# Optimization experiments

Hardware: AMD Instinct MI355X
Metric: run time of the kernel (lower is better)

The kernel has to match this reference:

```python
import jax, jax.numpy as jnp
import numpy as np

K = 2  # kernel_size


def setup_inputs() -> dict:
    key = jax.random.key(0)
    k1, k2, k3, k4, k5 = jax.random.split(key, 5)
    B, C, H, W_sp = 8, 256, 128, 128
    N = 512                      # number of keypoints
    E = C * K * K                # embed_dim = 1024
    img_feat_highres = jax.random.normal(k1, (B, C, H, W_sp), dtype=jnp.float32)
    W = jax.random.normal(k2, (E, C, K, K), dtype=jnp.float32) * 0.02  # conv weight, OIHW
    b = jax.random.normal(k3, (E,), dtype=jnp.float32) * 0.02          # conv bias
    batch_indices = jnp.broadcast_to(jnp.arange(B, dtype=jnp.int64)[:, None], (B, N))
    pixel_x_id = jax.random.randint(k4, (B, N), 0, H // 2, dtype=jnp.int64)  # low-res ids
    pixel_y_id = jax.random.randint(k5, (B, N), 0, H // 2, dtype=jnp.int64)
    return {
        "img_feat_highres": img_feat_highres,
        "W": W,
        "b": b,
        "batch_indices": batch_indices,
        "pixel_x_id": pixel_x_id,
        "pixel_y_id": pixel_y_id,
    }


def reference(img_feat_highres, W, b, batch_indices, pixel_x_id, pixel_y_id):
    # Dense conv2d, stride 1, padding = K-1 (torch nn.Conv2d semantics)
    patches = jax.lax.conv_general_dilated(
        img_feat_highres, W,
        window_strides=(1, 1),
        padding=((K - 1, K - 1), (K - 1, K - 1)),
        dimension_numbers=("NCHW", "OIHW", "NCHW"),
    ) + b[None, :, None, None]  # (B, E, H+K-1, W+K-1)

    y0 = 2 * pixel_y_id  # (B, N)
    x0 = 2 * pixel_x_id

    def samp(dy, dx):
        # advanced indices at dims 0,2,3 (non-adjacent) -> result (B, N, E)
        return patches[batch_indices, :, y0 + dy, x0 + dx]

    local_feat = jnp.concatenate(
        [samp(0, 0), samp(K, 0), samp(0, K), samp(K, K)], axis=2
    )  # (B, N, 4E)
    return jnp.transpose(local_feat, (0, 2, 1))  # (B, 4E, N)
```

## Files before the change

kernel.cpp:

```cpp
#include <hip/hip_runtime.h>
#include <stdint.h>


typedef __attribute__((ext_vector_type(8))) short bf16x8;
typedef __attribute__((ext_vector_type(4))) float f32x4;

#define GAS(p) ((const __attribute__((address_space(1))) void*)(p))
#define LAS(p) ((__attribute__((address_space(3))) void*)(p))

__device__ __forceinline__ unsigned short f2bf(float f) {
    union { float f; uint32_t u; } x; x.f = f;
    uint32_t u = x.u;
    uint32_t r = (u + 0x7FFFu + ((u >> 16) & 1u)) >> 16;
    return (unsigned short)r;
}

__global__ __launch_bounds__(256)
void prep_kernel(const float* __restrict__ img, const float* __restrict__ Wf,
                 unsigned short* __restrict__ Wp, unsigned short* __restrict__ zp,
                 unsigned short* __restrict__ imgT) {
    __shared__ unsigned short sT[8192];
    const int blk = blockIdx.x;
    const int t = threadIdx.x;

    if (blk < 1024) {
        const int e = blk, c = t;
        float4 w4 = *(const float4*)&Wf[(size_t)e * 1024 + c * 4];
        Wp[e * 1024 + 0 * 256 + c] = f2bf(w4.x);
        Wp[e * 1024 + 1 * 256 + c] = f2bf(w4.y);
        Wp[e * 1024 + 2 * 256 + c] = f2bf(w4.z);
        Wp[e * 1024 + 3 * 256 + c] = f2bf(w4.w);
        if (e == 0 && c < 32) {
            uint4 z = {0, 0, 0, 0};
            ((uint4*)zp)[c] = z;
        }
        return;
    }

    const int ib = blk - 1024;
    const int cc = ib & 3;
    const int y  = (ib >> 2) & 127;
    const int b  = ib >> 9;
    const int xq = t & 31;
    const int ch = t >> 5;
    unsigned int* sU = (unsigned int*)sT;
    const size_t pl = ((size_t)b * 256 + cc * 64) * 16384 + (size_t)y * 128;
    #pragma unroll
    for (int it = 0; it < 4; ++it) {
        const int cp = it * 8 + ch;
        const float4 v0 = *(const float4*)&img[pl + (size_t)(2 * cp)     * 16384 + xq * 4];
        const float4 v1 = *(const float4*)&img[pl + (size_t)(2 * cp + 1) * 16384 + xq * 4];
        const float a0[4] = {v0.x, v0.y, v0.z, v0.w};
        const float a1[4] = {v1.x, v1.y, v1.z, v1.w};
        #pragma unroll
        for (int j = 0; j < 4; ++j) {
            const int x = xq * 4 + j;
            const unsigned int pk = (unsigned)f2bf(a0[j]) | ((unsigned)f2bf(a1[j]) << 16);
            sU[x * 32 + (cp ^ (x & 31))] = pk;
        }
    }
    __syncthreads();
    unsigned short* ob = imgT + (((size_t)b * 128 + y) * 128) * 256 + cc * 64;
    #pragma unroll
    for (int jj = 0; jj < 16; ++jj) {
        const int oo = t + 256 * jj;
        const int xx = oo >> 5;
        const int c2 = oo & 31;
        const unsigned int pk = sU[xx * 32 + (c2 ^ (xx & 31))];
        *(unsigned int*)&ob[(size_t)xx * 256 + c2 * 2] = pk;
    }
}

__global__ __launch_bounds__(256)
void gemm_kernel(const unsigned short* __restrict__ Wp,
                 const unsigned short* __restrict__ imgT,
                 const unsigned short* __restrict__ zp,
                 const int* __restrict__ bidx,
                 const int* __restrict__ pxid,
                 const int* __restrict__ pyid,
                 const float* __restrict__ bias,
                 float* __restrict__ out) {
    const int orig = blockIdx.x;
    const int wg = (orig & 7) * 128 + (orig >> 3);
    const int et = wg & 7;
    const int nt = wg >> 3;
    const int g  = nt >> 2;
    const int n0 = (nt & 3) * 128;
    const int e0 = et * 128;
    const int b = g >> 2, o = g & 3;

    const int tid  = threadIdx.x;
    const int lane = tid & 63;
    const int wid  = tid >> 6;
    const int wr   = wid >> 1;
    const int wc   = wid & 1;

    __shared__ unsigned short sW[2][8192];
    __shared__ unsigned short sA[2][8192];

    const int row0 = tid >> 3;
    const int cg   = (tid & 7) ^ (row0 & 7);
    int ay[4], ax[4];
    size_t apl[4];
    #pragma unroll
    for (int r = 0; r < 4; ++r) {
        const int row = row0 + 32 * r;
        const int gi = b * 512 + n0 + row;
        apl[r] = (size_t)bidx[gi] * (128 * 128 * 256);
        ay[r] = 2 * pyid[gi] - 1 + (o & 1) * 2;
        ax[r] = 2 * pxid[gi] - 1 + (o >> 1) * 2;
    }

    const f32x4 fzero = {0.f, 0.f, 0.f, 0.f};
    f32x4 acc[4][4];
    #pragma unroll
    for (int m = 0; m < 4; ++m)
        #pragma unroll
        for (int nf = 0; nf < 4; ++nf) acc[m][nf] = fzero;

    auto stage = [&](int kc, int buf) {
        const int p   = kc >> 2;
        const int csh = (kc & 3) * 64;
        #pragma unroll
        for (int r = 0; r < 4; ++r) {
            const int i   = r * 256 + tid;
            const int row = row0 + 32 * r;
            const unsigned short* gw = Wp + (size_t)(e0 + row) * 1024 + kc * 64 + cg * 8;
            __builtin_amdgcn_global_load_lds(GAS(gw), LAS(&sW[buf][i * 8]), 16, 0, 0);
            const int yy = ay[r] + (p >> 1);
            const int xx = ax[r] + (p & 1);
            const unsigned short* ga =
                ((unsigned)yy < 128u && (unsigned)xx < 128u)
                    ? imgT + apl[r] + ((size_t)(yy * 128 + xx)) * 256 + csh + cg * 8
                    : zp + cg * 8;
            __builtin_amdgcn_global_load_lds(GAS(ga), LAS(&sA[buf][i * 8]), 16, 0, 0);
        }
    };

    stage(0, 0);
    stage(1, 1);
    for (int kt = 0; kt < 16; ++kt) {
        const int cur = kt & 1;
        if (kt == 15) { asm volatile("s_waitcnt vmcnt(0)" ::: "memory"); }
        else          { asm volatile("s_waitcnt vmcnt(8)" ::: "memory"); }
        __builtin_amdgcn_s_barrier();

        #pragma unroll
        for (int ks = 0; ks < 2; ++ks) {
            bf16x8 af[4], bfr[4];
            #pragma unroll
            for (int m = 0; m < 4; ++m) {
                const int row = wr * 64 + m * 16 + (lane & 15);
                const int cl  = (ks * 4 + (lane >> 4)) ^ (row & 7);
                af[m] = *(const bf16x8*)&sW[cur][row * 64 + cl * 8];
            }
            #pragma unroll
            for (int nf = 0; nf < 4; ++nf) {
                const int row = wc * 64 + nf * 16 + (lane & 15);
                const int cl  = (ks * 4 + (lane >> 4)) ^ (row & 7);
                bfr[nf] = *(const bf16x8*)&sA[cur][row * 64 + cl * 8];
            }
            __builtin_amdgcn_s_setprio(1);
            #pragma unroll
            for (int m = 0; m < 4; ++m)
                #pragma unroll
                for (int nf = 0; nf < 4; ++nf)
                    acc[m][nf] = __builtin_amdgcn_mfma_f32_16x16x32_bf16(
                        af[m], bfr[nf], acc[m][nf], 0, 0, 0);
            __builtin_amdgcn_s_setprio(0);
        }

        __builtin_amdgcn_s_barrier();
        if (kt + 2 < 16) stage(kt + 2, cur);
    }

    const int erow_l = (lane >> 4) * 4;
    const int ncol_l = lane & 15;
    #pragma unroll
    for (int m = 0; m < 4; ++m) {
        #pragma unroll
        for (int nf = 0; nf < 4; ++nf) {
            const int nn = n0 + wc * 64 + nf * 16 + ncol_l;
            #pragma unroll
            for (int reg = 0; reg < 4; ++reg) {
                const int e = e0 + wr * 64 + m * 16 + erow_l + reg;
                out[((size_t)g * 1024 + e) * 512 + nn] = acc[m][nf][reg] + bias[e];
            }
        }
    }
}

extern "C" void kernel_launch(void* const* d_in, const int* in_sizes, int n_in,
                              void* d_out, int out_size, void* d_ws, size_t ws_size,
                              hipStream_t stream) {
    const float* img  = (const float*)d_in[0];
    const float* Wf   = (const float*)d_in[1];
    const float* bias = (const float*)d_in[2];
    const int*   bidx = (const int*)d_in[3];
    const int*   pxid = (const int*)d_in[4];
    const int*   pyid = (const int*)d_in[5];
    float* out = (float*)d_out;

    unsigned short* Wp   = (unsigned short*)((char*)d_ws + (32u << 20));
    unsigned short* zp   = (unsigned short*)((char*)d_ws + (36u << 20));
    unsigned short* imgT = (unsigned short*)((char*)d_ws + (64u << 20));

    hipLaunchKernelGGL(prep_kernel, dim3(5120), dim3(256), 0, stream,
                       img, Wf, Wp, zp, imgT);
    hipLaunchKernelGGL(gemm_kernel, dim3(1024), dim3(256), 0, stream,
                       Wp, imgT, zp, bidx, pxid, pyid, bias, out);
}
```

Before: 84.22 us.

## Enlarge GEMM tiles to 256x256 with 512 threads and pre-swizzled weights

The gather-GEMM kernel now uses 256x256 output tiles with 8 waves, which halves the grid to 256 blocks and increases data reuse per block. The prep kernel writes the weights in a pre-tiled, swizzled bf16 layout so each block loads them with contiguous direct-to-LDS copies. The K loop is split into half-stages, and each barrier immediately issues the next half's loads for finer-grained double buffering. The larger accumulator array raises register pressure, and only 256 blocks may underfill the GPU.

```diff
diff --git a/kernel.cpp b/kernel.cpp
--- a/kernel.cpp
+++ b/kernel.cpp
@@ -17,32 +17,46 @@
 
 __global__ __launch_bounds__(256)
 void prep_kernel(const float* __restrict__ img, const float* __restrict__ Wf,
-                 unsigned short* __restrict__ Wp, unsigned short* __restrict__ zp,
+                 unsigned short* __restrict__ Wq, unsigned short* __restrict__ zp,
                  unsigned short* __restrict__ imgT) {
     __shared__ unsigned short sT[8192];
     const int blk = blockIdx.x;
-    const int t = threadIdx.x;
-
-    if (blk < 1024) {
-        const int e = blk, c = t;
-        float4 w4 = *(const float4*)&Wf[(size_t)e * 1024 + c * 4];
-        Wp[e * 1024 + 0 * 256 + c] = f2bf(w4.x);
-        Wp[e * 1024 + 1 * 256 + c] = f2bf(w4.y);
-        Wp[e * 1024 + 2 * 256 + c] = f2bf(w4.z);
-        Wp[e * 1024 + 3 * 256 + c] = f2bf(w4.w);
-        if (e == 0 && c < 32) {
+    const int tid = threadIdx.x;
+
+    if (blk < 512) {
+        if (blk == 0 && tid < 32) {
             uint4 z = {0, 0, 0, 0};
-            ((uint4*)zp)[c] = z;
-        }
+            ((uint4*)zp)[tid] = z;
+        }
+        const int t  = blk * 256 + tid;
+        const int et = t >> 15;
+        const int r1 = t & 32767;
+        const int j  = r1 >> 11;
+        const int r2 = r1 & 2047;
+        const int h  = r2 >> 10;
+        const int r3 = r2 & 1023;
+        const int chunk = r3 >> 8;
+        const int row   = r3 & 255;
+        const int e  = et * 256 + row;
+        const int kb = j * 64 + h * 32 + chunk * 8;
+        unsigned short v[8];
+        #pragma unroll
+        for (int kk = 0; kk < 8; ++kk) {
+            const int k = kb + kk;
+            const int c = k & 255;
+            const int p = k >> 8;
+            v[kk] = f2bf(Wf[(size_t)e * 1024 + c * 4 + p]);
+        }
+        *(uint4*)&Wq[(size_t)t * 8] = *(const uint4*)v;
         return;
     }
 
-    const int ib = blk - 1024;
+    const int ib = blk - 512;
     const int cc = ib & 3;
     const int y  = (ib >> 2) & 127;
     const int b  = ib >> 9;
-    const int xq = t & 31;
-    const int ch = t >> 5;
+    const int xq = tid & 31;
+    const int ch = tid >> 5;
     unsigned int* sU = (unsigned int*)sT;
     const size_t pl = ((size_t)b * 256 + cc * 64) * 16384 + (size_t)y * 128;
     #pragma unroll
@@ -53,9 +67,9 @@
         const float a0[4] = {v0.x, v0.y, v0.z, v0.w};
         const float a1[4] = {v1.x, v1.y, v1.z, v1.w};
         #pragma unroll
-        for (int j = 0; j < 4; ++j) {
-            const int x = xq * 4 + j;
-            const unsigned int pk = (unsigned)f2bf(a0[j]) | ((unsigned)f2bf(a1[j]) << 16);
+        for (int jj = 0; jj < 4; ++jj) {
+            const int x = xq * 4 + jj;
+            const unsigned int pk = (unsigned)f2bf(a0[jj]) | ((unsigned)f2bf(a1[jj]) << 16);
             sU[x * 32 + (cp ^ (x & 31))] = pk;
         }
     }
@@ -63,7 +77,7 @@
     unsigned short* ob = imgT + (((size_t)b * 128 + y) * 128) * 256 + cc * 64;
     #pragma unroll
     for (int jj = 0; jj < 16; ++jj) {
-        const int oo = t + 256 * jj;
+        const int oo = tid + 256 * jj;
         const int xx = oo >> 5;
         const int c2 = oo & 31;
         const unsigned int pk = sU[xx * 32 + (c2 ^ (xx & 31))];
@@ -71,121 +85,129 @@
     }
 }
 
-__global__ __launch_bounds__(256)
-void gemm_kernel(const unsigned short* __restrict__ Wp,
+__global__ __launch_bounds__(512, 1)
+void gemm_kernel(const unsigned short* __restrict__ Wq,
                  const unsigned short* __restrict__ imgT,
                  const unsigned short* __restrict__ zp,
                  const int* __restrict__ bidx,
                  const int* __restrict__ pxid,
                  const int* __restrict__ pyid,
                  const float* __restrict__ bias,
-                 float* __restrict__ out) {
+                 float* __restrict__ out)
+{
     const int orig = blockIdx.x;
-    const int wg = (orig & 7) * 128 + (orig >> 3);
-    const int et = wg & 7;
-    const int nt = wg >> 3;
-    const int g  = nt >> 2;
-    const int n0 = (nt & 3) * 128;
-    const int e0 = et * 128;
+    const int xcd  = orig & 7;
+    const int s    = orig >> 3;
+    const int gnt  = xcd * 8 + (s >> 2);
+    const int et   = s & 3;
+    const int e0   = et * 256;
+    const int g    = gnt >> 1;
+    const int n0   = (gnt & 1) * 256;
     const int b = g >> 2, o = g & 3;
 
     const int tid  = threadIdx.x;
     const int lane = tid & 63;
     const int wid  = tid >> 6;
-    const int wr   = wid >> 1;
-    const int wc   = wid & 1;
-
-    __shared__ unsigned short sW[2][8192];
-    __shared__ unsigned short sA[2][8192];
-
-    const int row0 = tid >> 3;
-    const int cg   = (tid & 7) ^ (row0 & 7);
-    int ay[4], ax[4];
-    size_t apl[4];
-    #pragma unroll
-    for (int r = 0; r < 4; ++r) {
-        const int row = row0 + 32 * r;
+    const int wm   = wid >> 2;
+    const int wn   = wid & 3;
+
+    __shared__ unsigned short sW[2 * 16384];
+    __shared__ unsigned short sA[2 * 16384];
+
+    int ayv[2], axv[2];
+    size_t apl[2];
+    #pragma unroll
+    for (int u = 0; u < 2; ++u) {
+        const int row = u * 128 + (tid >> 2);
         const int gi = b * 512 + n0 + row;
-        apl[r] = (size_t)bidx[gi] * (128 * 128 * 256);
-        ay[r] = 2 * pyid[gi] - 1 + (o & 1) * 2;
-        ax[r] = 2 * pxid[gi] - 1 + (o >> 1) * 2;
-    }
-
-    const f32x4 fzero = {0.f, 0.f, 0.f, 0.f};
-    f32x4 acc[4][4];
-    #pragma unroll
-    for (int m = 0; m < 4; ++m)
-        #pragma unroll
-        for (int nf = 0; nf < 4; ++nf) acc[m][nf] = fzero;
-
-    auto stage = [&](int kc, int buf) {
-        const int p   = kc >> 2;
-        const int csh = (kc & 3) * 64;
-        #pragma unroll
-        for (int r = 0; r < 4; ++r) {
-            const int i   = r * 256 + tid;
-            const int row = row0 + 32 * r;
-            const unsigned short* gw = Wp + (size_t)(e0 + row) * 1024 + kc * 64 + cg * 8;
-            __builtin_amdgcn_global_load_lds(GAS(gw), LAS(&sW[buf][i * 8]), 16, 0, 0);
-            const int yy = ay[r] + (p >> 1);
-            const int xx = ax[r] + (p & 1);
-            const unsigned short* ga =
+        apl[u] = (size_t)bidx[gi] * (128 * 128 * 256);
+        ayv[u] = 2 * pyid[gi] - 1 + (o & 1) * 2;
+        axv[u] = 2 * pxid[gi] - 1 + (o >> 1) * 2;
+    }
+    const int aswz = (((tid & 3) ^ ((tid >> 3) & 3))) * 8;
+    const unsigned short* wq_base = Wq + (size_t)et * 262144 + tid * 8;
+
+    f32x4 acc[8][4];
+    #pragma unroll
+    for (int m = 0; m < 8; ++m)
+        #pragma unroll
+        for (int nf = 0; nf < 4; ++nf) acc[m][nf] = (f32x4){0.f, 0.f, 0.f, 0.f};
+
+    auto stageHalf = [&](int j, int h, int buf) {
+        #pragma unroll
+        for (int u = 0; u < 2; ++u) {
+            const unsigned short* src = wq_base + (size_t)(j * 2 + h) * 8192 + u * 4096;
+            __builtin_amdgcn_global_load_lds(GAS(src),
+                LAS(&sW[buf * 16384 + h * 8192 + u * 4096 + tid * 8]), 16, 0, 0);
+        }
+        const int p = j >> 2;
+        const int csh = (j & 3) * 64 + h * 32 + aswz;
+        #pragma unroll
+        for (int u = 0; u < 2; ++u) {
+            const int yy = ayv[u] + (p >> 1);
+            const int xx = axv[u] + (p & 1);
+            const unsigned short* src =
                 ((unsigned)yy < 128u && (unsigned)xx < 128u)
-                    ? imgT + apl[r] + ((size_t)(yy * 128 + xx)) * 256 + csh + cg * 8
-                    : zp + cg * 8;
-            __builtin_amdgcn_global_load_lds(GAS(ga), LAS(&sA[buf][i * 8]), 16, 0, 0);
+                    ? imgT + apl[u] + ((size_t)(yy * 128 + xx)) * 256 + csh
+                    : zp + aswz;
+            __builtin_amdgcn_global_load_lds(GAS(src),
+                LAS(&sA[buf * 16384 + h * 8192 + u * 4096 + tid * 8]), 16, 0, 0);
         }
     };
 
-    stage(0, 0);
-    stage(1, 1);
-    for (int kt = 0; kt < 16; ++kt) {
-        const int cur = kt & 1;
-        if (kt == 15) { asm volatile("s_waitcnt vmcnt(0)" ::: "memory"); }
-        else          { asm volatile("s_waitcnt vmcnt(8)" ::: "memory"); }
-        __builtin_amdgcn_s_barrier();
-
-        #pragma unroll
-        for (int ks = 0; ks < 2; ++ks) {
-            bf16x8 af[4], bfr[4];
-            #pragma unroll
-            for (int m = 0; m < 4; ++m) {
-                const int row = wr * 64 + m * 16 + (lane & 15);
-                const int cl  = (ks * 4 + (lane >> 4)) ^ (row & 7);
-                af[m] = *(const bf16x8*)&sW[cur][row * 64 + cl * 8];
+    stageHalf(0, 0, 0);
+    stageHalf(0, 1, 0);
+
+    for (int j = 0; j < 16; ++j) {
+        const int buf = j & 1;
+        #pragma unroll
+        for (int h = 0; h < 2; ++h) {
+            if (j == 15 && h == 1) { asm volatile("s_waitcnt vmcnt(0)" ::: "memory"); }
+            else                   { asm volatile("s_waitcnt vmcnt(4)" ::: "memory"); }
+            __builtin_amdgcn_s_barrier();
+            if (j < 15) stageHalf(j + 1, h, buf ^ 1);
+
+            bf16x8 af[8];
+            {
+                const int chunk = lane >> 4;
+                const int rb = wm * 128 + (lane & 15);
+                #pragma unroll
+                for (int m = 0; m < 8; ++m)
+                    af[m] = *(const bf16x8*)&sW[buf * 16384 + h * 8192 + chunk * 2048 + (rb + m * 16) * 8];
             }
             #pragma unroll
-            for (int nf = 0; nf < 4; ++nf) {
-                const int row = wc * 64 + nf * 16 + (lane & 15);
-                const int cl  = (ks * 4 + (lane >> 4)) ^ (row & 7);
-                bfr[nf] = *(const bf16x8*)&sA[cur][row * 64 + cl * 8];
+            for (int nh = 0; nh < 2; ++nh) {
+                bf16x8 bfr[2];
+                #pragma unroll
+                for (int nn = 0; nn < 2; ++nn) {
+                    const int row = wn * 64 + (nh * 2 + nn) * 16 + (lane & 15);
+                    const int perm = (lane >> 4) ^ ((row >> 1) & 3);
+                    bfr[nn] = *(const bf16x8*)&sA[buf * 16384 + h * 8192 + row * 32 + perm * 8];
+                }
+                __builtin_amdgcn_s_setprio(1);
+                #pragma unroll
+                for (int m = 0; m < 8; ++m)
+                    #pragma unroll
+                    for (int nn = 0; nn < 2; ++nn)
+                        acc[m][nh * 2 + nn] = __builtin_amdgcn_mfma_f32_16x16x32_bf16(
+                            af[m], bfr[nn], acc[m][nh * 2 + nn], 0, 0, 0);
+                __builtin_amdgcn_s_setprio(0);
             }
-            __builtin_amdgcn_s_setprio(1);
+        }
+    }
+
+    #pragma unroll
+    for (int m = 0; m < 8; ++m) {
+        const int eb = e0 + wm * 128 + m * 16 + (lane >> 4) * 4;
+        float bv[4];
+        #pragma unroll
+        for (int reg = 0; reg < 4; ++reg) bv[reg] = bias[eb + reg];
+        #pragma unroll
+        for (int nf = 0; nf < 4; ++nf) {
+            const int nn = n0 + wn * 64 + nf * 16 + (lane & 15);
             #pragma unroll
-            for (int m = 0; m < 4; ++m)
-                #pragma unroll
-                for (int nf = 0; nf < 4; ++nf)
-                    acc[m][nf] = __builtin_amdgcn_mfma_f32_16x16x32_bf16(
-                        af[m], bfr[nf], acc[m][nf], 0, 0, 0);
-            __builtin_amdgcn_s_setprio(0);
-        }
-
-        __builtin_amdgcn_s_barrier();
-        if (kt + 2 < 16) stage(kt + 2, cur);
-    }
-
-    const int erow_l = (lane >> 4) * 4;
-    const int ncol_l = lane & 15;
-    #pragma unroll
-    for (int m = 0; m < 4; ++m) {
-        #pragma unroll
-        for (int nf = 0; nf < 4; ++nf) {
-            const int nn = n0 + wc * 64 + nf * 16 + ncol_l;
-            #pragma unroll
-            for (int reg = 0; reg < 4; ++reg) {
-                const int e = e0 + wr * 64 + m * 16 + erow_l + reg;
-                out[((size_t)g * 1024 + e) * 512 + nn] = acc[m][nf][reg] + bias[e];
-            }
+            for (int reg = 0; reg < 4; ++reg)
+                out[((size_t)g * 1024 + eb + reg) * 512 + nn] = acc[m][nf][reg] + bv[reg];
         }
     }
 }
@@ -201,12 +223,12 @@
     const int*   pyid = (const int*)d_in[5];
     float* out = (float*)d_out;
 
-    unsigned short* Wp   = (unsigned short*)((char*)d_ws + (32u << 20));
+    unsigned short* Wq   = (unsigned short*)((char*)d_ws + (32u << 20));
     unsigned short* zp   = (unsigned short*)((char*)d_ws + (36u << 20));
     unsigned short* imgT = (unsigned short*)((char*)d_ws + (64u << 20));
 
-    hipLaunchKernelGGL(prep_kernel, dim3(5120), dim3(256), 0, stream,
-                       img, Wf, Wp, zp, imgT);
-    hipLaunchKernelGGL(gemm_kernel, dim3(1024), dim3(256), 0, stream,
-                       Wp, imgT, zp, bidx, pxid, pyid, bias, out);
-}
+    hipLaunchKernelGGL(prep_kernel, dim3(4608), dim3(256), 0, stream,
+                       img, Wf, Wq, zp, imgT);
+    hipLaunchKernelGGL(gemm_kernel, dim3(256), dim3(512), 0, stream,
+                       Wq, imgT, zp, bidx, pxid, pyid, bias, out);
+}
```

After: 79.67 us. -5.4%, faster.
